# Kernel tuning notes

Measured on AMD Instinct MI355X. Metric: run time of the kernel, lower is better.

Reference implementation:

```python
import jax, jax.numpy as jnp
import numpy as np

N_HEAD = 16

def setup_inputs() -> dict:
    key = jax.random.key(0)
    ks = jax.random.split(key, 5)
    B, T, C = 2, 2048, 1024
    s = 1.0 / np.sqrt(C)
    return {
        "x": jax.random.normal(ks[0], (B, T, C), dtype=jnp.float32),
        "Wq": jax.random.normal(ks[1], (C, C), dtype=jnp.float32) * s,
        "Wk": jax.random.normal(ks[2], (C, C), dtype=jnp.float32) * s,
        "Wv": jax.random.normal(ks[3], (C, C), dtype=jnp.float32) * s,
        "Wo": jax.random.normal(ks[4], (C, C), dtype=jnp.float32) * s,
        "bo": jnp.zeros((C,), dtype=jnp.float32),
    }

def reference(x, Wq, Wk, Wv, Wo, bo):
    B, T, C = x.shape
    H = N_HEAD
    D = C // H

    def shape(t):  # (B,T,C) -> (B,H,T,D)
        return t.reshape(B, T, H, D).transpose(0, 2, 1, 3)

    q = shape(x @ Wq)
    k = shape(x @ Wk)
    v = shape(x @ Wv)

    # scores: (B,H,T,Tk), Tk == T (no past_kv)
    att = jnp.einsum("bhtd,bhsd->bhts", q, k) * (1.0 / np.sqrt(D))
    i = jnp.arange(T)[:, None]
    j = jnp.arange(T)[None, :]
    causal = (j <= i)  # (T, Tk)
    att = jnp.where(causal[None, None], att, -jnp.inf)
    att = jax.nn.softmax(att, axis=-1)  # dropout=0.0 -> identity

    out = jnp.einsum("bhts,bhsd->bhtd", att, v)
    out = out.transpose(0, 2, 1, 3).reshape(B, T, C)
    out = out @ Wo + bo
    return out, (k, v)
```

## Files before the change

kernel.cpp:

```cpp
#include <hip/hip_runtime.h>
#include <hip/hip_bf16.h>

constexpr int B_ = 2;
constexpr int T_ = 2048;
constexpr int C_ = 1024;
constexpr int H_ = 16;
constexpr int D_ = 64;
constexpr int M_ = B_ * T_;

typedef __attribute__((ext_vector_type(8))) short bf16x8;
typedef __attribute__((ext_vector_type(4))) float f32x4;
typedef const __attribute__((address_space(1))) void gaddr_t;
typedef __attribute__((address_space(3))) void laddr_t;

__device__ __forceinline__ unsigned short f2bf(float f) {
    unsigned u = __float_as_uint(f);
    return (unsigned short)((u + 0x7fffu + ((u >> 16) & 1u)) >> 16);
}

union BF8 { bf16x8 v; __hip_bfloat162 h[4]; };

__device__ __forceinline__ bf16x8 cvt8(const float4 a, const float4 b) {
    BF8 r;
    r.h[0] = __float22bfloat162_rn(make_float2(a.x, a.y));
    r.h[1] = __float22bfloat162_rn(make_float2(a.z, a.w));
    r.h[2] = __float22bfloat162_rn(make_float2(b.x, b.y));
    r.h[3] = __float22bfloat162_rn(make_float2(b.z, b.w));
    return r.v;
}

__global__ __launch_bounds__(256)
void prep(const float* __restrict__ x, const float* __restrict__ Wq,
          const float* __restrict__ Wk, const float* __restrict__ Wv,
          const float* __restrict__ Wo, unsigned short* __restrict__ xb,
          unsigned short* __restrict__ wtb)
{
    const int z = blockIdx.z;
    const int tid = threadIdx.x;

    if (z == 4) {
        const int base = (blockIdx.y * 16 + blockIdx.x) * 4096 + tid;
#pragma unroll
        for (int i = 0; i < 16; ++i) {
            const int idx = base + i * 256;
            float4 v = ((const float4*)x)[idx];
            union { __hip_bfloat162 h[2]; ushort4 u; } o;
            o.h[0] = __float22bfloat162_rn(make_float2(v.x, v.y));
            o.h[1] = __float22bfloat162_rn(make_float2(v.z, v.w));
            ((ushort4*)xb)[idx] = o.u;
        }
        return;
    }

    __shared__ float tile[64][65];
    const float* W = (z == 0) ? Wq : (z == 1) ? Wk : (z == 2) ? Wv : Wo;
    unsigned short* O = wtb + (size_t)z * C_ * C_;

    const int n0 = blockIdx.x * 64, k0 = blockIdx.y * 64;
    const int r = tid >> 4, c4 = (tid & 15) * 4;

#pragma unroll
    for (int i = 0; i < 4; ++i) {
        const int kk = i * 16 + r;
        float4 v = *(const float4*)(W + (size_t)(k0 + kk) * C_ + n0 + c4);
        tile[c4 + 0][kk] = v.x;
        tile[c4 + 1][kk] = v.y;
        tile[c4 + 2][kk] = v.z;
        tile[c4 + 3][kk] = v.w;
    }
    __syncthreads();
#pragma unroll
    for (int i = 0; i < 4; ++i) {
        const int nn = i * 16 + r;
        ushort4 o;
        o.x = f2bf(tile[nn][c4 + 0]);
        o.y = f2bf(tile[nn][c4 + 1]);
        o.z = f2bf(tile[nn][c4 + 2]);
        o.w = f2bf(tile[nn][c4 + 3]);
        *(ushort4*)(O + (size_t)(n0 + nn) * C_ + k0 + c4) = o;
    }
}

template<int WRITE_KB>
__global__ __launch_bounds__(512)
void gemm_qkv(const unsigned short* __restrict__ xb, const unsigned short* __restrict__ wtb,
              unsigned short* __restrict__ qb, float* __restrict__ kout,
              float* __restrict__ vout, unsigned short* __restrict__ kb,
              unsigned short* __restrict__ vtt)
{
    __shared__ unsigned short As[2][128 * 64];
    __shared__ unsigned short Bs[2][192 * 64];

    const int tid = threadIdx.x;
    const int n0g = blockIdx.x * 192;
    const int m0 = blockIdx.y * 128;

    const int lane = tid & 63, w = tid >> 6;
    const int wm = (w >> 2) * 64, wn = (w & 3) * 48;
    const int fr = lane & 15, qd = lane >> 4;

    int arow[2], aofs[2]; size_t alds[2];
#pragma unroll
    for (int cc = 0; cc < 2; ++cc) {
        const int c = tid + cc * 512;
        arow[cc] = c >> 3;
        aofs[cc] = ((c & 7) ^ (arow[cc] & 7)) * 8;
        alds[cc] = (size_t)c * 16;
    }
    int brow[3], bofs[3]; size_t blds[3];
#pragma unroll
    for (int cc = 0; cc < 3; ++cc) {
        const int c = tid + cc * 512;
        brow[cc] = c >> 3;
        bofs[cc] = ((c & 7) ^ (brow[cc] & 7)) * 8;
        blds[cc] = (size_t)c * 16;
    }

#define STAGE(s, kt)                                                                   \
    {                                                                                  \
        _Pragma("unroll")                                                              \
        for (int cc = 0; cc < 2; ++cc)                                                 \
            __builtin_amdgcn_global_load_lds(                                          \
                (gaddr_t*)(xb + (size_t)(m0 + arow[cc]) * C_ + (kt) * 64 + aofs[cc]),  \
                (laddr_t*)((char*)As[s] + alds[cc]), 16, 0, 0);                        \
        _Pragma("unroll")                                                              \
        for (int cc = 0; cc < 3; ++cc)                                                 \
            __builtin_amdgcn_global_load_lds(                                          \
                (gaddr_t*)(wtb + (size_t)(n0g + brow[cc]) * C_ + (kt) * 64 + bofs[cc]),\
                (laddr_t*)((char*)Bs[s] + blds[cc]), 16, 0, 0);                        \
    }

    f32x4 acc[4][3] = {};
    constexpr int NT = C_ / 64;

    STAGE(0, 0);
    asm volatile("s_waitcnt vmcnt(0)" ::: "memory");
    __builtin_amdgcn_s_barrier();
    __builtin_amdgcn_sched_barrier(0);

    for (int t = 0; t < NT; ++t) {
        const int s = t & 1;
        if (t + 1 < NT) STAGE(s ^ 1, t + 1);

        const unsigned short* Ac = As[s];
        const unsigned short* Bc = Bs[s];
#pragma unroll
        for (int half = 0; half < 2; ++half) {
            bf16x8 af[4], bfv[3];
#pragma unroll
            for (int mt = 0; mt < 4; ++mt) {
                const int row = wm + mt * 16 + fr, dg = half * 4 + qd;
                af[mt] = *(const bf16x8*)&Ac[row * 64 + ((dg ^ (row & 7)) * 8)];
            }
#pragma unroll
            for (int nt = 0; nt < 3; ++nt) {
                const int row = wn + nt * 16 + fr, dg = half * 4 + qd;
                bfv[nt] = *(const bf16x8*)&Bc[row * 64 + ((dg ^ (row & 7)) * 8)];
            }
#pragma unroll
            for (int mt = 0; mt < 4; ++mt)
#pragma unroll
                for (int nt = 0; nt < 3; ++nt)
                    acc[mt][nt] = __builtin_amdgcn_mfma_f32_16x16x32_bf16(
                        bfv[nt], af[mt], acc[mt][nt], 0, 0, 0);
        }

        asm volatile("s_waitcnt vmcnt(0)" ::: "memory");
        __builtin_amdgcn_s_barrier();
        __builtin_amdgcn_sched_barrier(0);
    }
#undef STAGE

#pragma unroll
    for (int mt = 0; mt < 4; ++mt) {
        const int mm = m0 + wm + mt * 16 + fr;
        const int b = mm >> 11, t = mm & (T_ - 1);
#pragma unroll
        for (int nt = 0; nt < 3; ++nt) {
            const int nn = n0g + wn + nt * 16 + qd * 4;
            const int which = nn >> 10;
            const int nw = nn & 1023;
            const int h = nw >> 6, d0 = nw & 63;
            const int bh = b * H_ + h;
            const size_t off = ((size_t)bh * T_ + t) * D_ + d0;
            const f32x4 a4 = acc[mt][nt];
            if (which == 0) {
                *(ushort4*)(qb + off) =
                    make_ushort4(f2bf(a4[0]), f2bf(a4[1]), f2bf(a4[2]), f2bf(a4[3]));
            } else if (which == 1) {
                *(float4*)(kout + off) = make_float4(a4[0], a4[1], a4[2], a4[3]);
                if (WRITE_KB)
                    *(ushort4*)(kb + off) =
                        make_ushort4(f2bf(a4[0]), f2bf(a4[1]), f2bf(a4[2]), f2bf(a4[3]));
            } else {
                *(float4*)(vout + off) = make_float4(a4[0], a4[1], a4[2], a4[3]);
                unsigned short* vb = vtt
                    + (((size_t)bh * (T_ / 64) + (t >> 6)) * 64 + d0) * 64 + (t & 63);
#pragma unroll
                for (int r = 0; r < 4; ++r) vb[(size_t)r * 64] = f2bf(a4[r]);
            }
        }
    }
}

__global__ __launch_bounds__(512)
void gemm_o(const unsigned short* __restrict__ ab, const unsigned short* __restrict__ wot,
            const float* __restrict__ bo, float* __restrict__ out)
{
    __shared__ unsigned short As[3][128 * 64];
    __shared__ unsigned short Bs[3][128 * 64];

    const int tid = threadIdx.x;
    const int n0 = blockIdx.x * 128;
    const int m0 = blockIdx.y * 128;

    const int lane = tid & 63, w = tid >> 6;
    const int wm = (w >> 2) * 64, wn2 = (w & 3) * 32;
    const int fr = lane & 15, qd = lane >> 4;

    int crow[2], cofs[2]; size_t clds[2];
#pragma unroll
    for (int cc = 0; cc < 2; ++cc) {
        const int c = tid + cc * 512;
        crow[cc] = c >> 3;
        cofs[cc] = ((c & 7) ^ (crow[cc] & 7)) * 8;
        clds[cc] = (size_t)c * 16;
    }

#define STAGE_O(s, kt)                                                             \
    {                                                                              \
        _Pragma("unroll")                                                          \
        for (int cc = 0; cc < 2; ++cc) {                                           \
            __builtin_amdgcn_global_load_lds(                                      \
                (gaddr_t*)(ab + (size_t)(m0 + crow[cc]) * C_ + (kt) * 64 + cofs[cc]),  \
                (laddr_t*)((char*)As[s] + clds[cc]), 16, 0, 0);                    \
            __builtin_amdgcn_global_load_lds(                                      \
                (gaddr_t*)(wot + (size_t)(n0 + crow[cc]) * C_ + (kt) * 64 + cofs[cc]), \
                (laddr_t*)((char*)Bs[s] + clds[cc]), 16, 0, 0);                    \
        }                                                                          \
    }

    f32x4 acc[4][2] = {};
    constexpr int NT = C_ / 64;

    STAGE_O(0, 0);
    STAGE_O(1, 1);
    asm volatile("s_waitcnt vmcnt(4)" ::: "memory");
    __builtin_amdgcn_s_barrier();
    __builtin_amdgcn_sched_barrier(0);

    for (int t = 0; t < NT; ++t) {
        const int s = t % 3;
        if (t + 2 < NT) STAGE_O((t + 2) % 3, t + 2);

        const unsigned short* Ac = As[s];
        const unsigned short* Bc = Bs[s];
#pragma unroll
        for (int half = 0; half < 2; ++half) {
            bf16x8 af[4], bfv[2];
#pragma unroll
            for (int mt = 0; mt < 4; ++mt) {
                const int row = wm + mt * 16 + fr, dg = half * 4 + qd;
                af[mt] = *(const bf16x8*)&Ac[row * 64 + ((dg ^ (row & 7)) * 8)];
            }
#pragma unroll
            for (int nt = 0; nt < 2; ++nt) {
                const int row = wn2 + nt * 16 + fr, dg = half * 4 + qd;
                bfv[nt] = *(const bf16x8*)&Bc[row * 64 + ((dg ^ (row & 7)) * 8)];
            }
#pragma unroll
            for (int mt = 0; mt < 4; ++mt)
#pragma unroll
                for (int nt = 0; nt < 2; ++nt)
                    acc[mt][nt] = __builtin_amdgcn_mfma_f32_16x16x32_bf16(
                        bfv[nt], af[mt], acc[mt][nt], 0, 0, 0);
        }

        if (t + 2 < NT)      asm volatile("s_waitcnt vmcnt(4)" ::: "memory");
        else if (t + 1 < NT) asm volatile("s_waitcnt vmcnt(0)" ::: "memory");
        __builtin_amdgcn_s_barrier();
        __builtin_amdgcn_sched_barrier(0);
    }
#undef STAGE_O

#pragma unroll
    for (int mt = 0; mt < 4; ++mt) {
        const int mm = m0 + wm + mt * 16 + fr;
#pragma unroll
        for (int nt = 0; nt < 2; ++nt) {
            const int nn = n0 + wn2 + nt * 16 + qd * 4;
            const float4 b4 = *(const float4*)(bo + nn);
            *(float4*)(out + (size_t)mm * C_ + nn) =
                make_float4(acc[mt][nt][0] + b4.x, acc[mt][nt][1] + b4.y,
                            acc[mt][nt][2] + b4.z, acc[mt][nt][3] + b4.w);
        }
    }
}

__global__ __launch_bounds__(256)
void attn_lds(const unsigned short* __restrict__ qb, const unsigned short* __restrict__ kb,
              const unsigned short* __restrict__ vtt, unsigned short* __restrict__ attb)
{
    __shared__ unsigned short Ks[2][64 * 64];
    __shared__ unsigned short Vs[2][64 * 64];
    __shared__ alignas(16) unsigned short Pt[4][16 * 72];

    const int tid = threadIdx.x;
    const int lane = tid & 63, w = tid >> 6;
    const int fr = lane & 15, qd = lane >> 4;

    const int blk = blockIdx.x;
    const int xcd = blk & 7, within = blk >> 3;
    const int bh = xcd * 4 + (within & 3);
    const int jj = within >> 2;
    const int kk_ = jj >> 3, ii_ = jj & 7;
    const int qt = (kk_ == 0) ? (31 - ii_) : (kk_ == 1) ? ii_
                 : (kk_ == 2) ? (23 - ii_) : (8 + ii_);
    const int b = bh >> 4, h = bh & 15;

    unsigned short* Pw = Pt[w];
    const unsigned short* qB = qb  + (size_t)bh * T_ * D_;
    const unsigned short* kB = kb  + (size_t)bh * T_ * D_;
    const unsigned short* vT = vtt + (size_t)bh * (T_ / 64) * 64 * 64;

    const int qr0 = qt * 64 + w * 16;
    const int qrow_g = qr0 + fr;

    bf16x8 aq0 = *(const bf16x8*)(qB + (size_t)(qr0 + fr) * D_ + qd * 8);
    bf16x8 aq1 = *(const bf16x8*)(qB + (size_t)(qr0 + fr) * D_ + 32 + qd * 8);

    f32x4 accT[4] = {};
    float l_i = 0.0f;
    const float sc2 = 0.18033688f;

    const int L0 = w * 128 + lane, L1 = L0 + 64;
    const int r0 = L0 >> 3, e0 = (((L0 & 7) ^ (r0 & 7)) * 8);
    const int r1 = L1 >> 3, e1 = (((L1 & 7) ^ (r1 & 7)) * 8);

    {
        __builtin_amdgcn_global_load_lds((gaddr_t*)(kB + r0 * 64 + e0),
            (laddr_t*)((char*)Ks[0] + (size_t)L0 * 16), 16, 0, 0);
        __builtin_amdgcn_global_load_lds((gaddr_t*)(kB + r1 * 64 + e1),
            (laddr_t*)((char*)Ks[0] + (size_t)L1 * 16), 16, 0, 0);
        __builtin_amdgcn_global_load_lds((gaddr_t*)(vT + r0 * 64 + e0),
            (laddr_t*)((char*)Vs[0] + (size_t)L0 * 16), 16, 0, 0);
        __builtin_amdgcn_global_load_lds((gaddr_t*)(vT + r1 * 64 + e1),
            (laddr_t*)((char*)Vs[0] + (size_t)L1 * 16), 16, 0, 0);
    }
    asm volatile("s_waitcnt vmcnt(0)" ::: "memory");
    __builtin_amdgcn_s_barrier();
    __builtin_amdgcn_sched_barrier(0);

    for (int jt = 0; jt <= qt; ++jt) {
        const int cur = jt & 1;
        if (jt < qt) {
            const unsigned short* kt = kB + (size_t)((jt + 1) * 64) * 64;
            const unsigned short* vt = vT + (size_t)(jt + 1) * 4096;
            char* Kn = (char*)Ks[cur ^ 1];
            char* Vn = (char*)Vs[cur ^ 1];
            __builtin_amdgcn_global_load_lds((gaddr_t*)(kt + r0 * 64 + e0),
                (laddr_t*)(Kn + (size_t)L0 * 16), 16, 0, 0);
            __builtin_amdgcn_global_load_lds((gaddr_t*)(kt + r1 * 64 + e1),
                (laddr_t*)(Kn + (size_t)L1 * 16), 16, 0, 0);
            __builtin_amdgcn_global_load_lds((gaddr_t*)(vt + r0 * 64 + e0),
                (laddr_t*)(Vn + (size_t)L0 * 16), 16, 0, 0);
            __builtin_amdgcn_global_load_lds((gaddr_t*)(vt + r1 * 64 + e1),
                (laddr_t*)(Vn + (size_t)L1 * 16), 16, 0, 0);
        }
        const unsigned short* Kc = Ks[cur];
        const unsigned short* Vc = Vs[cur];

        bf16x8 bk[8];
#pragma unroll
        for (int q8 = 0; q8 < 8; ++q8) {
            const int row = (q8 >> 1) * 16 + fr;
            const int dg = (q8 & 1) * 4 + qd;
            bk[q8] = *(const bf16x8*)&Kc[row * 64 + ((dg ^ (row & 7)) * 8)];
        }

        f32x4 s4[4] = {};
        __builtin_amdgcn_s_setprio(1);
#pragma unroll
        for (int nt = 0; nt < 4; ++nt) {
            s4[nt] = __builtin_amdgcn_mfma_f32_16x16x32_bf16(bk[nt * 2 + 0], aq0, s4[nt], 0, 0, 0);
            s4[nt] = __builtin_amdgcn_mfma_f32_16x16x32_bf16(bk[nt * 2 + 1], aq1, s4[nt], 0, 0, 0);
        }
        __builtin_amdgcn_s_setprio(0);

        if (jt == qt) {
            const int kbase = jt * 64 + qd * 4;
#pragma unroll
            for (int nt = 0; nt < 4; ++nt)
#pragma unroll
            for (int r = 0; r < 4; ++r) {
                const int kcol = kbase + nt * 16 + r;
                const float pv = (kcol <= qrow_g)
                               ? __builtin_amdgcn_exp2f(s4[nt][r] * sc2) : 0.0f;
                s4[nt][r] = pv;
                l_i += pv;
            }
        } else {
#pragma unroll
            for (int nt = 0; nt < 4; ++nt)
#pragma unroll
            for (int r = 0; r < 4; ++r) {
                const float pv = __builtin_amdgcn_exp2f(s4[nt][r] * sc2);
                s4[nt][r] = pv;
                l_i += pv;
            }
        }

#pragma unroll
        for (int nt = 0; nt < 4; ++nt) {
            union { __hip_bfloat162 h2[2]; unsigned long long u; } pk;
            pk.h2[0] = __float22bfloat162_rn(make_float2(s4[nt][0], s4[nt][1]));
            pk.h2[1] = __float22bfloat162_rn(make_float2(s4[nt][2], s4[nt][3]));
            *(unsigned long long*)&Pw[fr * 72 + nt * 16 + qd * 4] = pk.u;
        }
        const bf16x8 ap0 = *(const bf16x8*)&Pw[fr * 72 + qd * 8];
        const bf16x8 ap1 = *(const bf16x8*)&Pw[fr * 72 + 32 + qd * 8];

        bf16x8 bv[8];
#pragma unroll
        for (int q8 = 0; q8 < 8; ++q8) {
            const int row = (q8 >> 1) * 16 + fr;
            const int dg = (q8 & 1) * 4 + qd;
            bv[q8] = *(const bf16x8*)&Vc[row * 64 + ((dg ^ (row & 7)) * 8)];
        }

        __builtin_amdgcn_s_setprio(1);
#pragma unroll
        for (int nt = 0; nt < 4; ++nt) {
            accT[nt] = __builtin_amdgcn_mfma_f32_16x16x32_bf16(bv[nt * 2 + 0], ap0, accT[nt], 0, 0, 0);
            accT[nt] = __builtin_amdgcn_mfma_f32_16x16x32_bf16(bv[nt * 2 + 1], ap1, accT[nt], 0, 0, 0);
        }
        __builtin_amdgcn_s_setprio(0);

        asm volatile("s_waitcnt vmcnt(0)" ::: "memory");
        __builtin_amdgcn_s_barrier();
        __builtin_amdgcn_sched_barrier(0);
    }

    l_i += __shfl_xor(l_i, 16);
    l_i += __shfl_xor(l_i, 32);
    const float inv = 1.0f / l_i;

#pragma unroll
    for (int nt = 0; nt < 4; ++nt) {
        union { __hip_bfloat162 h2[2]; unsigned long long u; } ok;
        ok.h2[0] = __float22bfloat162_rn(make_float2(accT[nt][0] * inv, accT[nt][1] * inv));
        ok.h2[1] = __float22bfloat162_rn(make_float2(accT[nt][2] * inv, accT[nt][3] * inv));
        *(unsigned long long*)&Pw[fr * 72 + nt * 16 + qd * 4] = ok.u;
    }
    {
        const int row = lane >> 2, d0 = (lane & 3) * 16;
        const bf16x8 o0 = *(const bf16x8*)&Pw[row * 72 + d0];
        const bf16x8 o1 = *(const bf16x8*)&Pw[row * 72 + d0 + 8];
        unsigned short* op = attb + ((size_t)b * T_ + qr0 + row) * C_ + h * 64 + d0;
        *(bf16x8*)op = o0;
        *(bf16x8*)(op + 8) = o1;
    }
}

__global__ __launch_bounds__(256)
void attn_v4(const unsigned short* __restrict__ qb, const float* __restrict__ kf,
             const unsigned short* __restrict__ vtt, unsigned short* __restrict__ attb)
{
    __shared__ alignas(16) unsigned short Pt[4][16 * 72];

    const int tid = threadIdx.x;
    const int lane = tid & 63, w = tid >> 6;
    const int fr = lane & 15, qd = lane >> 4;

    const int blk = blockIdx.x;
    const int xcd = blk & 7, within = blk >> 3;
    const int bh = xcd * 4 + (within & 3);
    const int jj = within >> 2;
    const int kk_ = jj >> 3, ii_ = jj & 7;
    const int qt = (kk_ == 0) ? (31 - ii_) : (kk_ == 1) ? ii_
                 : (kk_ == 2) ? (23 - ii_) : (8 + ii_);
    const int b = bh >> 4, h = bh & 15;

    unsigned short* Pw = Pt[w];
    const unsigned short* qB = qb  + (size_t)bh * T_ * D_;
    const float*          kB = kf  + (size_t)bh * T_ * D_;
    const unsigned short* vT = vtt + (size_t)bh * (T_ / 64) * 64 * 64;

    const int qr0 = qt * 64 + w * 16;
    const int qrow_g = qr0 + fr;

    bf16x8 aq0 = *(const bf16x8*)(qB + (size_t)(qr0 + fr) * D_ + qd * 8);
    bf16x8 aq1 = *(const bf16x8*)(qB + (size_t)(qr0 + fr) * D_ + 32 + qd * 8);

    f32x4 accT[4] = {};
    float l_i = 0.0f;
    const float sc2 = 0.18033688f;

    for (int jt = 0; jt <= qt; ++jt) {
        bf16x8 bk[8];
#pragma unroll
        for (int q8 = 0; q8 < 8; ++q8) {
            const float* p = kB + (size_t)(jt * 64 + (q8 >> 1) * 16 + fr) * D_
                           + (q8 & 1) * 32 + qd * 8;
            bk[q8] = cvt8(*(const float4*)p, *(const float4*)(p + 4));
        }
        f32x4 s4[4] = {};
#pragma unroll
        for (int nt = 0; nt < 4; ++nt) {
            s4[nt] = __builtin_amdgcn_mfma_f32_16x16x32_bf16(bk[nt * 2 + 0], aq0, s4[nt], 0, 0, 0);
            s4[nt] = __builtin_amdgcn_mfma_f32_16x16x32_bf16(bk[nt * 2 + 1], aq1, s4[nt], 0, 0, 0);
        }
        if (jt == qt) {
            const int kbase = jt * 64 + qd * 4;
#pragma unroll
            for (int nt = 0; nt < 4; ++nt)
#pragma unroll
            for (int r = 0; r < 4; ++r) {
                const int kcol = kbase + nt * 16 + r;
                const float pv = (kcol <= qrow_g)
                               ? __builtin_amdgcn_exp2f(s4[nt][r] * sc2) : 0.0f;
                s4[nt][r] = pv; l_i += pv;
            }
        } else {
#pragma unroll
            for (int nt = 0; nt < 4; ++nt)
#pragma unroll
            for (int r = 0; r < 4; ++r) {
                const float pv = __builtin_amdgcn_exp2f(s4[nt][r] * sc2);
                s4[nt][r] = pv; l_i += pv;
            }
        }
#pragma unroll
        for (int nt = 0; nt < 4; ++nt) {
            union { __hip_bfloat162 h2[2]; unsigned long long u; } pk;
            pk.h2[0] = __float22bfloat162_rn(make_float2(s4[nt][0], s4[nt][1]));
            pk.h2[1] = __float22bfloat162_rn(make_float2(s4[nt][2], s4[nt][3]));
            *(unsigned long long*)&Pw[fr * 72 + nt * 16 + qd * 4] = pk.u;
        }
        const bf16x8 ap0 = *(const bf16x8*)&Pw[fr * 72 + qd * 8];
        const bf16x8 ap1 = *(const bf16x8*)&Pw[fr * 72 + 32 + qd * 8];

        bf16x8 bv[8];
#pragma unroll
        for (int q8 = 0; q8 < 8; ++q8)
            bv[q8] = *(const bf16x8*)(vT + (size_t)jt * 4096
                                      + ((q8 >> 1) * 16 + fr) * 64 + (q8 & 1) * 32 + qd * 8);
#pragma unroll
        for (int nt = 0; nt < 4; ++nt) {
            accT[nt] = __builtin_amdgcn_mfma_f32_16x16x32_bf16(bv[nt * 2 + 0], ap0, accT[nt], 0, 0, 0);
            accT[nt] = __builtin_amdgcn_mfma_f32_16x16x32_bf16(bv[nt * 2 + 1], ap1, accT[nt], 0, 0, 0);
        }
    }

    l_i += __shfl_xor(l_i, 16);
    l_i += __shfl_xor(l_i, 32);
    const float inv = 1.0f / l_i;
#pragma unroll
    for (int nt = 0; nt < 4; ++nt) {
        union { __hip_bfloat162 h2[2]; unsigned long long u; } ok;
        ok.h2[0] = __float22bfloat162_rn(make_float2(accT[nt][0] * inv, accT[nt][1] * inv));
        ok.h2[1] = __float22bfloat162_rn(make_float2(accT[nt][2] * inv, accT[nt][3] * inv));
        *(unsigned long long*)&Pw[fr * 72 + nt * 16 + qd * 4] = ok.u;
    }
    {
        const int row = lane >> 2, d0 = (lane & 3) * 16;
        const bf16x8 o0 = *(const bf16x8*)&Pw[row * 72 + d0];
        const bf16x8 o1 = *(const bf16x8*)&Pw[row * 72 + d0 + 8];
        unsigned short* op = attb + ((size_t)b * T_ + qr0 + row) * C_ + h * 64 + d0;
        *(bf16x8*)op = o0;
        *(bf16x8*)(op + 8) = o1;
    }
}

extern "C" void kernel_launch(void* const* d_in, const int* in_sizes, int n_in,
                              void* d_out, int out_size, void* d_ws, size_t ws_size,
                              hipStream_t stream)
{
    (void)in_sizes; (void)n_in; (void)out_size;
    const float* x  = (const float*)d_in[0];
    const float* Wq = (const float*)d_in[1];
    const float* Wk = (const float*)d_in[2];
    const float* Wv = (const float*)d_in[3];
    const float* Wo = (const float*)d_in[4];
    const float* bo = (const float*)d_in[5];

    float* out  = (float*)d_out;
    float* kout = out  + (size_t)M_ * C_;
    float* vout = kout + (size_t)B_ * H_ * T_ * D_;

    unsigned short* xb   = (unsigned short*)d_ws;
    unsigned short* wtb  = xb  + (size_t)M_ * C_;
    unsigned short* qb   = wtb + (size_t)4 * C_ * C_;
    unsigned short* vtt  = qb  + (size_t)M_ * C_;
    unsigned short* kb   = vtt + (size_t)M_ * C_;
    unsigned short* attb = xb;
    const bool use_kb = ws_size >= (size_t)40 * 1024 * 1024;

    prep<<<dim3(16, 16, 5), 256, 0, stream>>>(x, Wq, Wk, Wv, Wo, xb, wtb);

    if (use_kb)
        gemm_qkv<1><<<dim3(16, 32), 512, 0, stream>>>(xb, wtb, qb, kout, vout, kb, vtt);
    else
        gemm_qkv<0><<<dim3(16, 32), 512, 0, stream>>>(xb, wtb, qb, kout, vout, kb, vtt);

    if (use_kb)
        attn_lds<<<1024, 256, 0, stream>>>(qb, kb, vtt, attb);
    else
        attn_v4<<<1024, 256, 0, stream>>>(qb, kout, vtt, attb);

    gemm_o<<<dim3(8, 32), 512, 0, stream>>>(attb, wtb + (size_t)3 * C_ * C_, bo, out);
}
```

Baseline: 181.0 us.

## Fold softmax scale into Q, compute row sums via MFMA, simplify tile order

```diff
diff --git a/kernel.cpp b/kernel.cpp
--- a/kernel.cpp
+++ b/kernel.cpp
@@ -171,6 +171,7 @@
     }
 #undef STAGE
 
+    const float SC2 = 0.18033688f;
 #pragma unroll
     for (int mt = 0; mt < 4; ++mt) {
         const int mm = m0 + wm + mt * 16 + fr;
@@ -186,7 +187,8 @@
             const f32x4 a4 = acc[mt][nt];
             if (which == 0) {
                 *(ushort4*)(qb + off) =
-                    make_ushort4(f2bf(a4[0]), f2bf(a4[1]), f2bf(a4[2]), f2bf(a4[3]));
+                    make_ushort4(f2bf(a4[0] * SC2), f2bf(a4[1] * SC2),
+                                 f2bf(a4[2] * SC2), f2bf(a4[3] * SC2));
             } else if (which == 1) {
                 *(float4*)(kout + off) = make_float4(a4[0], a4[1], a4[2], a4[3]);
                 if (WRITE_KB)
@@ -313,9 +315,7 @@
     const int xcd = blk & 7, within = blk >> 3;
     const int bh = xcd * 4 + (within & 3);
     const int jj = within >> 2;
-    const int kk_ = jj >> 3, ii_ = jj & 7;
-    const int qt = (kk_ == 0) ? (31 - ii_) : (kk_ == 1) ? ii_
-                 : (kk_ == 2) ? (23 - ii_) : (8 + ii_);
+    const int qt = 31 - jj;
     const int b = bh >> 4, h = bh & 15;
 
     unsigned short* Pw = Pt[w];
@@ -329,9 +329,12 @@
     bf16x8 aq0 = *(const bf16x8*)(qB + (size_t)(qr0 + fr) * D_ + qd * 8);
     bf16x8 aq1 = *(const bf16x8*)(qB + (size_t)(qr0 + fr) * D_ + 32 + qd * 8);
 
+    const short one_bf = (short)0x3F80;
+    const bf16x8 ones8 = {one_bf, one_bf, one_bf, one_bf,
+                          one_bf, one_bf, one_bf, one_bf};
+
     f32x4 accT[4] = {};
-    float l_i = 0.0f;
-    const float sc2 = 0.18033688f;
+    f32x4 accL = {};
 
     const int L0 = w * 128 + lane, L1 = L0 + 64;
     const int r0 = L0 >> 3, e0 = (((L0 & 7) ^ (r0 & 7)) * 8);
@@ -394,20 +397,15 @@
 #pragma unroll
             for (int r = 0; r < 4; ++r) {
                 const int kcol = kbase + nt * 16 + r;
-                const float pv = (kcol <= qrow_g)
-                               ? __builtin_amdgcn_exp2f(s4[nt][r] * sc2) : 0.0f;
-                s4[nt][r] = pv;
-                l_i += pv;
+                s4[nt][r] = (kcol <= qrow_g)
+                          ? __builtin_amdgcn_exp2f(s4[nt][r]) : 0.0f;
             }
         } else {
 #pragma unroll
             for (int nt = 0; nt < 4; ++nt)
 #pragma unroll
-            for (int r = 0; r < 4; ++r) {
-                const float pv = __builtin_amdgcn_exp2f(s4[nt][r] * sc2);
-                s4[nt][r] = pv;
-                l_i += pv;
-            }
+            for (int r = 0; r < 4; ++r)
+                s4[nt][r] = __builtin_amdgcn_exp2f(s4[nt][r]);
         }
 
 #pragma unroll
@@ -434,6 +432,8 @@
             accT[nt] = __builtin_amdgcn_mfma_f32_16x16x32_bf16(bv[nt * 2 + 0], ap0, accT[nt], 0, 0, 0);
             accT[nt] = __builtin_amdgcn_mfma_f32_16x16x32_bf16(bv[nt * 2 + 1], ap1, accT[nt], 0, 0, 0);
         }
+        accL = __builtin_amdgcn_mfma_f32_16x16x32_bf16(ones8, ap0, accL, 0, 0, 0);
+        accL = __builtin_amdgcn_mfma_f32_16x16x32_bf16(ones8, ap1, accL, 0, 0, 0);
         __builtin_amdgcn_s_setprio(0);
 
         asm volatile("s_waitcnt vmcnt(0)" ::: "memory");
@@ -441,9 +441,7 @@
         __builtin_amdgcn_sched_barrier(0);
     }
 
-    l_i += __shfl_xor(l_i, 16);
-    l_i += __shfl_xor(l_i, 32);
-    const float inv = 1.0f / l_i;
+    const float inv = 1.0f / accL[0];
 
 #pragma unroll
     for (int nt = 0; nt < 4; ++nt) {
@@ -494,7 +492,6 @@
 
     f32x4 accT[4] = {};
     float l_i = 0.0f;
-    const float sc2 = 0.18033688f;
 
     for (int jt = 0; jt <= qt; ++jt) {
         bf16x8 bk[8];
@@ -518,7 +515,7 @@
             for (int r = 0; r < 4; ++r) {
                 const int kcol = kbase + nt * 16 + r;
                 const float pv = (kcol <= qrow_g)
-                               ? __builtin_amdgcn_exp2f(s4[nt][r] * sc2) : 0.0f;
+                               ? __builtin_amdgcn_exp2f(s4[nt][r]) : 0.0f;
                 s4[nt][r] = pv; l_i += pv;
             }
         } else {
@@ -526,7 +523,7 @@
             for (int nt = 0; nt < 4; ++nt)
 #pragma unroll
             for (int r = 0; r < 4; ++r) {
-                const float pv = __builtin_amdgcn_exp2f(s4[nt][r] * sc2);
+                const float pv = __builtin_amdgcn_exp2f(s4[nt][r]);
                 s4[nt][r] = pv; l_i += pv;
             }
         }
```

Measured after the change: 177.6 us (median of 2 runs). Within noise of the previous version (-1.9%).
